# Kernel tuning notes

Measured on AMD Instinct MI355X. Metric: run time of the kernel, lower is better.

## Reference

```python
import jax, jax.numpy as jnp
import numpy as np

# Dimensions
T = 1024      # tokens
D = 1024      # d_model
DFF = 1024    # expert intermediate dim
R = 64        # tucker rank (r_in == r_out)
G = 8         # n_group
E = 32        # experts_per_group
NEXP = G * E  # 256 routed experts
K = 8         # top-k


def setup_inputs() -> dict:
    key = jax.random.key(0)
    ks = jax.random.split(key, 12)
    s = 0.02
    return {
        "x": jax.random.normal(ks[0], (T, D), jnp.float32),
        "Wg": jax.random.normal(ks[1], (D, NEXP), jnp.float32) * s,
        "uin_gate": jax.random.normal(ks[2], (G, D, R), jnp.float32) * s,
        "core_gate": jax.random.normal(ks[3], (G, E, R, R), jnp.float32) * s,
        "uout_gate": jax.random.normal(ks[4], (G, R, DFF), jnp.float32) * s,
        "uin_up": jax.random.normal(ks[5], (G, D, R), jnp.float32) * s,
        "core_up": jax.random.normal(ks[6], (G, E, R, R), jnp.float32) * s,
        "uout_up": jax.random.normal(ks[7], (G, R, DFF), jnp.float32) * s,
        "uin_down": jax.random.normal(ks[8], (G, DFF, R), jnp.float32) * s,
        "core_down": jax.random.normal(ks[9], (G, E, R, R), jnp.float32) * s,
        "uout_down": jax.random.normal(ks[10], (G, R, D), jnp.float32) * s,
    }


def _moe_forward(x, Wg, uin_gate, core_gate, uout_gate,
                 uin_up, core_up, uout_up,
                 uin_down, core_down, uout_down):
    Tn, d = x.shape
    # Router: top-k over 256 experts, softmax over the k logits (fp32 as in torch)
    logits = x @ Wg                                   # [T, NEXP]
    w, sel = jax.lax.top_k(logits, K)                 # [T, K]
    w = jax.nn.softmax(w.astype(jnp.float32), axis=-1).astype(x.dtype)

    e = sel.reshape(-1)                               # [F] global expert id
    g = e // E                                        # [F] group id
    tok = jnp.repeat(jnp.arange(Tn), K)               # [F] source token id
    mask = (g[:, None] == jnp.arange(G)[None, :]).astype(x.dtype)  # [F, G]

    def gather_in(uin):
        # project tokens with every group's u_in once, then gather per pair
        pre = jnp.einsum('td,gdr->gtr', x, uin)       # [G, T, R]
        return pre[g, tok]                            # [F, R]

    def core_apply(xin, core):
        # per-pair Tucker core slice bmm: x.unsqueeze(1) @ core[rel_idx]
        slices = core.reshape(G * E, R, R)[e]         # [F, R, R] gather
        return jnp.einsum('fr,fro->fo', xin, slices)  # [F, R]

    def group_out(h, U):
        # per-pair group-specific projection: h[f] @ U[g_f]
        out = jnp.zeros((h.shape[0], U.shape[-1]), h.dtype)
        for gi in range(G):  # fixed small loop over 8 groups
            out = out + (h * mask[:, gi:gi + 1]) @ U[gi]
        return out

    gate_h = group_out(core_apply(gather_in(uin_gate), core_gate), uout_gate)  # [F, DFF]
    up_h = group_out(core_apply(gather_in(uin_up), core_up), uout_up)          # [F, DFF]
    act = jax.nn.silu(gate_h) * up_h                                           # SwiGLU
    xin_d = group_out(act, uin_down)                                           # [F, R]
    out_f = group_out(core_apply(xin_d, core_down), uout_down)                 # [F, D]
    out_f = out_f * w.reshape(-1)[:, None]
    # scatter-add expert outputs back to tokens
    return jax.ops.segment_sum(out_f, tok, num_segments=Tn)


def reference(x, Wg, uin_gate, core_gate, uout_gate,
              uin_up, core_up, uout_up,
              uin_down, core_down, uout_down):
    return _moe_forward(x, Wg, uin_gate, core_gate, uout_gate,
                        uin_up, core_up, uout_up,
                        uin_down, core_down, uout_down)
```

## Files before the change

### kernel.cpp

```cpp
#include <hip/hip_runtime.h>
#include <hip/hip_bf16.h>
#include <math.h>


#define T_ 1024
#define D_ 1024
#define DFF_ 1024
#define R_ 64
#define G_ 8
#define E_ 32
#define NEXP_ 256
#define K_ 8
#define F_ 8192
#define LKZ_ 4
#define LTB_ 8
#define PKZ_ 2
#define DKZ_ 4
#define LP_ 72

typedef short bf16x8 __attribute__((ext_vector_type(8)));
typedef float f32x4 __attribute__((ext_vector_type(4)));

__device__ __forceinline__ unsigned short f2bf(float f) {
  unsigned int u = __float_as_uint(f);
  u += 0x7fffu + ((u >> 16) & 1u);
  return (unsigned short)(u >> 16);
}

__device__ __forceinline__ void stage_tile(short* dst, const unsigned short* src,
                                           int gp, int tid) {
  for (int idx = tid; idx < 512; idx += 256) {
    int r = idx >> 3, c8 = (idx & 7) << 3;
    *(uint4*)&dst[r * LP_ + c8] = *(const uint4*)&src[(size_t)r * gp + c8];
  }
}

__device__ __forceinline__ void stage_tile_guard(short* dst, const unsigned short* src,
                                                 int gp, int rows_valid, int tid) {
  for (int idx = tid; idx < 512; idx += 256) {
    int r = idx >> 3, c8 = (idx & 7) << 3;
    uint4 v = make_uint4(0u, 0u, 0u, 0u);
    if (r < rows_valid) v = *(const uint4*)&src[(size_t)r * gp + c8];
    *(uint4*)&dst[r * LP_ + c8] = v;
  }
}

__device__ __forceinline__ void stage_tile_f32(short* dst, const float* src,
                                               int gp, int tid) {
  for (int idx = tid; idx < 512; idx += 256) {
    int r = idx >> 3, c8 = (idx & 7) << 3;
    const float* s = &src[(size_t)r * gp + c8];
    float4 v0 = *(const float4*)s;
    float4 v1 = *(const float4*)(s + 4);
    uint4 u;
    u.x = ((unsigned)f2bf(v0.y) << 16) | f2bf(v0.x);
    u.y = ((unsigned)f2bf(v0.w) << 16) | f2bf(v0.z);
    u.z = ((unsigned)f2bf(v1.y) << 16) | f2bf(v1.x);
    u.w = ((unsigned)f2bf(v1.w) << 16) | f2bf(v1.z);
    *(uint4*)&dst[r * LP_ + c8] = u;
  }
}

__device__ __forceinline__ void mma_strip(const short* As, const short* Bs,
                                          int ms, int lane, f32x4* acc) {
  int lm = lane & 15;
  int lk = (lane >> 4) << 3;
#pragma unroll
  for (int kc = 0; kc < 64; kc += 32) {
    bf16x8 a = *(const bf16x8*)&As[(ms + lm) * LP_ + kc + lk];
#pragma unroll
    for (int nt = 0; nt < 4; ++nt) {
      bf16x8 b = *(const bf16x8*)&Bs[(nt * 16 + lm) * LP_ + kc + lk];
      acc[nt] = __builtin_amdgcn_mfma_f32_16x16x32_bf16(a, b, acc[nt], 0, 0, 0);
    }
  }
}

__global__ __launch_bounds__(256) void k_prep_logits(
    const float* __restrict__ x, const float* __restrict__ Wg,
    const float* __restrict__ s0, const float* __restrict__ s1,
    const float* __restrict__ s2, const float* __restrict__ s3,
    const float* __restrict__ s4, const float* __restrict__ s5,
    unsigned short* __restrict__ xb,
    unsigned short* __restrict__ d0, unsigned short* __restrict__ d1,
    unsigned short* __restrict__ d2, unsigned short* __restrict__ d3,
    unsigned short* __restrict__ d4, unsigned short* __restrict__ d5,
    int* __restrict__ cnt, int* __restrict__ tickets, float* __restrict__ Yf,
    float* __restrict__ lp) {
  __shared__ float shbuf[64 * 65];
  int b = blockIdx.x;
  if (b < 512) {
    int t0 = (b & 127) * LTB_;
    int z = b >> 7;
    int e = threadIdx.x;
    float* xs = shbuf;
    float a[LTB_] = {};
    int dc = z * 256;
    {
      int idx = threadIdx.x * 8;
      int tl = idx >> 8, d = idx & 255;
      *(float4*)&xs[tl * 256 + d] = *(const float4*)&x[(size_t)(t0 + tl) * D_ + dc + d];
      *(float4*)&xs[tl * 256 + d + 4] = *(const float4*)&x[(size_t)(t0 + tl) * D_ + dc + d + 4];
    }
    __syncthreads();
#pragma unroll 2
    for (int d2 = 0; d2 < 256; d2 += 4) {
      float w0 = Wg[(size_t)(dc + d2 + 0) * NEXP_ + e];
      float w1 = Wg[(size_t)(dc + d2 + 1) * NEXP_ + e];
      float w2 = Wg[(size_t)(dc + d2 + 2) * NEXP_ + e];
      float w3 = Wg[(size_t)(dc + d2 + 3) * NEXP_ + e];
#pragma unroll
      for (int j = 0; j < LTB_; ++j) {
        float4 xv = *(const float4*)&xs[j * 256 + d2];
        float aj = a[j];
        aj = fmaf(xv.x, w0, aj);
        aj = fmaf(xv.y, w1, aj);
        aj = fmaf(xv.z, w2, aj);
        aj = fmaf(xv.w, w3, aj);
        a[j] = aj;
      }
    }
    size_t base = (size_t)z * T_ * NEXP_;
#pragma unroll
    for (int j = 0; j < LTB_; ++j)
      lp[base + (size_t)(t0 + j) * NEXP_ + e] = a[j];
    return;
  }
  int b2 = b - 512;
  int id = b2 >> 7, rem = b2 & 127, g = rem >> 4, tile = rem & 15;
  if (id == 6) {
    size_t base = ((size_t)g * 16 + tile) * 8192;
    for (int i = threadIdx.x; i < 2048; i += 256) {
      size_t idx = base + (size_t)i * 4;
      float4 v = *(const float4*)&x[idx];
      xb[idx + 0] = f2bf(v.x);
      xb[idx + 1] = f2bf(v.y);
      xb[idx + 2] = f2bf(v.z);
      xb[idx + 3] = f2bf(v.w);
    }
    size_t ybase = ((size_t)g * 16 + tile) * 4096;
    float4 z4 = make_float4(0.f, 0.f, 0.f, 0.f);
    for (int i = threadIdx.x; i < 1024; i += 256)
      *(float4*)&Yf[ybase + (size_t)i * 4] = z4;
    if (g == 0 && tile == 0) {
      cnt[threadIdx.x] = 0;
      if (threadIdx.x == 0) tickets[0] = 0;
    }
    return;
  }
  const float* src = id == 0 ? s0 : id == 1 ? s1 : id == 2 ? s2 : id == 3 ? s3 : id == 4 ? s4 : s5;
  unsigned short* dst = id == 0 ? d0 : id == 1 ? d1 : id == 2 ? d2 : id == 3 ? d3 : id == 4 ? d4 : d5;
  if (id < 3) {
    int r0 = tile * 64;
    for (int idx = threadIdx.x; idx < 4096; idx += 256) {
      int r = idx >> 6, c = idx & 63;
      shbuf[r * 65 + c] = src[((size_t)g * 1024 + r0 + r) * 64 + c];
    }
    __syncthreads();
    for (int idx = threadIdx.x; idx < 4096; idx += 256) {
      int c = idx >> 6, r = idx & 63;
      dst[((size_t)g * 64 + c) * 1024 + r0 + r] = f2bf(shbuf[r * 65 + c]);
    }
  } else {
    int c0 = tile * 64;
    for (int idx = threadIdx.x; idx < 4096; idx += 256) {
      int r = idx >> 6, c = idx & 63;
      shbuf[r * 65 + c] = src[((size_t)g * 64 + r) * 1024 + c0 + c];
    }
    __syncthreads();
    if (id == 5) {
      for (int idx = threadIdx.x; idx < 4096; idx += 256) {
        int c = idx >> 6, r = idx & 63;
        dst[(size_t)(c0 + c) * 512 + g * 64 + r] = f2bf(shbuf[r * 65 + c]);
      }
    } else {
      for (int idx = threadIdx.x; idx < 4096; idx += 256) {
        int c = idx >> 6, r = idx & 63;
        dst[((size_t)g * 1024 + c0 + c) * 64 + r] = f2bf(shbuf[r * 65 + c]);
      }
    }
  }
}

__global__ __launch_bounds__(256) void k_pre_topk(
    const unsigned short* __restrict__ xb,
    const unsigned short* __restrict__ uinT_g, const unsigned short* __restrict__ uinT_u,
    const float* __restrict__ lp,
    float* __restrict__ Pgp, float* __restrict__ Pup,
    float* __restrict__ wsm, int* __restrict__ bucket, int* __restrict__ cnt,
    int* __restrict__ tickets, int* __restrict__ off) {
  __shared__ short sh2[2 * 64 * LP_];
  __shared__ int lastfl;
  int b = blockIdx.x;
  int tid = threadIdx.x;
  if (b >= 256) {
    int b2 = b - 256;
    int tile = b2 & 15, g = (b2 >> 4) & 7, zz = b2 >> 7;
    int gu = zz >> 1, kz = zz & 1;
    const unsigned short* U = gu ? uinT_u : uinT_g;
    float* P = gu ? Pup : Pgp;
    int t0 = tile * 64;
    short* As = sh2;
    short* Bs = sh2 + 64 * LP_;
    int lane = tid & 63, ms = (tid >> 6) * 16;
    f32x4 acc[4] = {};
    int dlo = kz * (D_ / PKZ_);
    for (int dc = dlo; dc < dlo + D_ / PKZ_; dc += 64) {
      stage_tile(As, xb + (size_t)t0 * D_ + dc, D_, tid);
      stage_tile(Bs, U + (size_t)g * 64 * 1024 + dc, 1024, tid);
      __syncthreads();
      mma_strip(As, Bs, ms, lane, acc);
      __syncthreads();
    }
    int lm = lane & 15, lq = (lane >> 4) * 4;
#pragma unroll
    for (int nt = 0; nt < 4; ++nt)
#pragma unroll
      for (int r = 0; r < 4; ++r)
        P[((size_t)(kz * G_ + g) * T_ + t0 + ms + lq + r) * R_ + nt * 16 + lm] = acc[nt][r];
    return;
  }
  int wave = tid >> 6;
  int lane = tid & 63;
  int t = b * 4 + wave;
  float v[4];
  int idx[4];
#pragma unroll
  for (int j = 0; j < 4; ++j) {
    idx[j] = lane + 64 * j;
    float s = 0.f;
#pragma unroll
    for (int z = 0; z < LKZ_; ++z)
      s += lp[(size_t)z * T_ * NEXP_ + (size_t)t * NEXP_ + idx[j]];
    v[j] = s;
  }
  float topv[K_];
  int topi[K_];
#pragma unroll
  for (int k = 0; k < K_; ++k) {
    float bv = v[0];
    int bi = idx[0];
#pragma unroll
    for (int j = 1; j < 4; ++j)
      if (v[j] > bv || (v[j] == bv && idx[j] < bi)) { bv = v[j]; bi = idx[j]; }
#pragma unroll
    for (int o2 = 32; o2 > 0; o2 >>= 1) {
      float ov = __shfl_xor(bv, o2);
      int oi = __shfl_xor(bi, o2);
      if (ov > bv || (ov == bv && oi < bi)) { bv = ov; bi = oi; }
    }
    topv[k] = bv;
    topi[k] = bi;
#pragma unroll
    for (int j = 0; j < 4; ++j)
      if (idx[j] == bi) v[j] = -INFINITY;
  }
  float m = topv[0];
  float ev[K_];
  float s = 0.f;
#pragma unroll
  for (int k = 0; k < K_; ++k) { ev[k] = expf(topv[k] - m); s += ev[k]; }
  float inv = 1.f / s;
  if (lane < K_) {
    wsm[t * K_ + lane] = ev[lane] * inv;
    int r1 = atomicAdd(&cnt[topi[lane]], 1);
    bucket[topi[lane] * 1024 + r1] = t * K_ + lane;
  }
  __threadfence();
  __syncthreads();
  if (tid == 0) lastfl = (atomicAdd(&tickets[0], 1) == 255) ? 1 : 0;
  __syncthreads();
  if (lastfl) {
    int* sarr = (int*)sh2;
    int i = tid;
    int c0 = atomicAdd(&cnt[i], 0);
    sarr[i] = c0;
    __syncthreads();
    for (int d = 1; d < NEXP_; d <<= 1) {
      int vv = (i >= d) ? sarr[i - d] : 0;
      __syncthreads();
      sarr[i] += vv;
      __syncthreads();
    }
    off[i + 1] = sarr[i];
    if (i == 0) off[0] = 0;
  }
}

__global__ __launch_bounds__(256) void k_core_gu(const float* __restrict__ Pgp,
                                                 const float* __restrict__ Pup,
                                                 const float* __restrict__ core_g,
                                                 const float* __restrict__ core_u,
                                                 const int* __restrict__ bucket,
                                                 const int* __restrict__ off,
                                                 unsigned short* __restrict__ xgb,
                                                 unsigned short* __restrict__ xub) {
  int e = blockIdx.x >> 1, half = blockIdx.x & 1;
  int g = e >> 5;
  __shared__ float cg[4096], cu[4096];
  __shared__ float rg[4][64], ru[4][64];
  int tid = threadIdx.x;
  for (int i = tid; i < 1024; i += 256) {
    *(float4*)&cg[i * 4] = *(const float4*)&core_g[(size_t)e * 4096 + (size_t)i * 4];
    *(float4*)&cu[i * 4] = *(const float4*)&core_u[(size_t)e * 4096 + (size_t)i * 4];
  }
  int p0 = off[e], n = off[e + 1] - p0;
  if (n < 0) n = 0;
  if (n > 1024) n = 1024;
  int hn = (n + 1) >> 1;
  int i0 = half * hn;
  int i1 = i0 + hn; if (i1 > n) i1 = n;
  int pl = tid >> 6, o = tid & 63;
  __syncthreads();
  for (int ib = i0; ib < i1; ib += 4) {
    int i = ib + pl;
    bool valid = i < i1;
    int p = p0 + i;
    float sg = 0.f, su = 0.f;
    if (valid) {
      int t = bucket[e * 1024 + i] >> 3;
#pragma unroll
      for (int kz = 0; kz < PKZ_; ++kz) {
        sg += Pgp[((size_t)(kz * G_ + g) * T_ + t) * R_ + o];
        su += Pup[((size_t)(kz * G_ + g) * T_ + t) * R_ + o];
      }
    }
    __syncthreads();
    rg[pl][o] = sg;
    ru[pl][o] = su;
    __syncthreads();
    if (valid) {
      float ag = 0.f, au = 0.f;
#pragma unroll 8
      for (int r = 0; r < R_; ++r) {
        ag = fmaf(rg[pl][r], cg[r * R_ + o], ag);
        au = fmaf(ru[pl][r], cu[r * R_ + o], au);
      }
      xgb[(size_t)p * R_ + o] = f2bf(ag);
      xub[(size_t)p * R_ + o] = f2bf(au);
    }
  }
}

__global__ __launch_bounds__(256) void k_fused_ad(const unsigned short* __restrict__ xgb,
                                                  const unsigned short* __restrict__ xub,
                                                  const unsigned short* __restrict__ uoutT_g,
                                                  const unsigned short* __restrict__ uoutT_u,
                                                  const unsigned short* __restrict__ uinT_d,
                                                  const int* __restrict__ off,
                                                  float* __restrict__ xdp) {
  int g = blockIdx.y;
  int kz = blockIdx.z;
  int p0 = off[g * E_];
  int pend = off[g * E_ + E_];
  if (p0 < 0) p0 = 0;
  if (pend > F_) pend = F_;
  if (pend < p0) pend = p0;
  int ntiles = (pend - p0 + 63) >> 6;
  __shared__ short Ag[64 * LP_], Au[64 * LP_];
  __shared__ short Bg[64 * LP_], Bu[64 * LP_], Bd[64 * LP_];
  __shared__ short Pt[64 * LP_];
  int tid = threadIdx.x, lane = tid & 63, ms = (tid >> 6) * 16;
  int lm = lane & 15, lq = (lane >> 4) * 4;
  for (int tile = blockIdx.x; tile < ntiles; tile += gridDim.x) {
    int pbase = p0 + tile * 64;
    int rv = pend - pbase; if (rv > 64) rv = 64;
    stage_tile_guard(Ag, xgb + (size_t)pbase * R_, R_, rv, tid);
    stage_tile_guard(Au, xub + (size_t)pbase * R_, R_, rv, tid);
    f32x4 accd[4] = {};
#pragma unroll
    for (int c4 = 0; c4 < 4; ++c4) {
      int cc = kz * (DFF_ / DKZ_) + c4 * 64;
      stage_tile(Bg, uoutT_g + ((size_t)g * DFF_ + cc) * R_, R_, tid);
      stage_tile(Bu, uoutT_u + ((size_t)g * DFF_ + cc) * R_, R_, tid);
      stage_tile(Bd, uinT_d + (size_t)g * 64 * 1024 + cc, 1024, tid);
      __syncthreads();
      f32x4 accg[4] = {}, accu[4] = {};
      mma_strip(Ag, Bg, ms, lane, accg);
      mma_strip(Au, Bu, ms, lane, accu);
#pragma unroll
      for (int nt = 0; nt < 4; ++nt)
#pragma unroll
        for (int r = 0; r < 4; ++r) {
          float gv = accg[nt][r];
          float av = gv / (1.f + expf(-gv)) * accu[nt][r];
          Pt[(ms + lq + r) * LP_ + nt * 16 + lm] = (short)f2bf(av);
        }
      mma_strip(Pt, Bd, ms, lane, accd);
      __syncthreads();
    }
#pragma unroll
    for (int nt = 0; nt < 4; ++nt)
#pragma unroll
      for (int r = 0; r < 4; ++r) {
        int p = pbase + ms + lq + r;
        if (p < pend) xdp[((size_t)kz * F_ + p) * R_ + nt * 16 + lm] = accd[nt][r];
      }
    __syncthreads();
  }
}

__global__ __launch_bounds__(256) void k_down_core(const float* __restrict__ xdp,
                                                   const float* __restrict__ core_d,
                                                   const int* __restrict__ bucket,
                                                   const float* __restrict__ wsm,
                                                   const int* __restrict__ off,
                                                   float* __restrict__ Yf) {
  int e = blockIdx.x >> 1, half = blockIdx.x & 1;
  int g = e >> 5;
  __shared__ float cd[4096];
  __shared__ float xs[4][64];
  int tid = threadIdx.x;
  for (int i = tid; i < 1024; i += 256)
    *(float4*)&cd[i * 4] = *(const float4*)&core_d[(size_t)e * 4096 + (size_t)i * 4];
  int p0 = off[e], n = off[e + 1] - p0;
  if (n < 0) n = 0;
  if (n > 1024) n = 1024;
  int hn = (n + 1) >> 1;
  int i0 = half * hn;
  int i1 = i0 + hn; if (i1 > n) i1 = n;
  int pl = tid >> 6, o = tid & 63;
  __syncthreads();
  for (int ib = i0; ib < i1; ib += 4) {
    int i = ib + pl;
    bool valid = i < i1;
    int p = p0 + i;
    int f = valid ? bucket[e * 1024 + i] : 0;
    float s = 0.f;
    if (valid) {
#pragma unroll
      for (int kz = 0; kz < DKZ_; ++kz) s += xdp[((size_t)kz * F_ + p) * R_ + o];
    }
    __syncthreads();
    xs[pl][o] = s;
    __syncthreads();
    if (valid) {
      float a = 0.f;
#pragma unroll 8
      for (int r = 0; r < R_; ++r) a = fmaf(xs[pl][r], cd[r * R_ + o], a);
      atomicAdd(&Yf[(size_t)(f >> 3) * 512 + g * 64 + o], wsm[f] * a);
    }
  }
}

__global__ __launch_bounds__(256) void k_fin(const float* __restrict__ Yf,
                                             const unsigned short* __restrict__ Uod2T,
                                             float* __restrict__ out) {
  int t0 = blockIdx.x * 64;
  int d0 = blockIdx.y * 64;
  __shared__ short As[64 * LP_], Bs[64 * LP_];
  __shared__ float Os[64 * 68];
  int tid = threadIdx.x, lane = tid & 63, ms = (tid >> 6) * 16;
  int lm = lane & 15, lq = (lane >> 4) * 4;
  f32x4 acc[4] = {};
  for (int kc = 0; kc < 512; kc += 64) {
    stage_tile_f32(As, Yf + (size_t)t0 * 512 + kc, 512, tid);
    stage_tile(Bs, Uod2T + (size_t)d0 * 512 + kc, 512, tid);
    __syncthreads();
    mma_strip(As, Bs, ms, lane, acc);
    __syncthreads();
  }
#pragma unroll
  for (int nt = 0; nt < 4; ++nt)
#pragma unroll
    for (int r = 0; r < 4; ++r)
      Os[(ms + lq + r) * 68 + nt * 16 + lm] = acc[nt][r];
  __syncthreads();
  for (int idx = tid; idx < 1024; idx += 256) {
    int r = idx >> 4, c4 = (idx & 15) << 2;
    *(float4*)&out[(size_t)(t0 + r) * D_ + d0 + c4] = *(const float4*)&Os[r * 68 + c4];
  }
}

extern "C" void kernel_launch(void* const* d_in, const int* in_sizes, int n_in,
                              void* d_out, int out_size, void* d_ws, size_t ws_size,
                              hipStream_t stream) {
  const float* x = (const float*)d_in[0];
  const float* Wg = (const float*)d_in[1];
  const float* uin_gate = (const float*)d_in[2];
  const float* core_gate = (const float*)d_in[3];
  const float* uout_gate = (const float*)d_in[4];
  const float* uin_up = (const float*)d_in[5];
  const float* core_up = (const float*)d_in[6];
  const float* uout_up = (const float*)d_in[7];
  const float* uin_down = (const float*)d_in[8];
  const float* core_down = (const float*)d_in[9];
  const float* uout_down = (const float*)d_in[10];
  float* out = (float*)d_out;

  char* ws = (char*)d_ws;
  size_t o = 0;
  auto alloc = [&](size_t bytes) { size_t r = o; o = (o + bytes + 255) & ~(size_t)255; return r; };
  size_t o_lp = alloc((size_t)LKZ_ * T_ * NEXP_ * 4);
  size_t o_wsm = alloc(F_ * 4);
  size_t o_bucket = alloc((size_t)NEXP_ * 1024 * 4);
  size_t o_cnt = alloc(NEXP_ * 4);
  size_t o_tickets = alloc(256);
  size_t o_off = alloc((NEXP_ + 1) * 4);
  size_t o_xb = alloc((size_t)T_ * D_ * 2);
  size_t o_uinT_g = alloc((size_t)G_ * 64 * 1024 * 2);
  size_t o_uinT_u = alloc((size_t)G_ * 64 * 1024 * 2);
  size_t o_uinT_d = alloc((size_t)G_ * 64 * 1024 * 2);
  size_t o_uoutT_g = alloc((size_t)G_ * 1024 * 64 * 2);
  size_t o_uoutT_u = alloc((size_t)G_ * 1024 * 64 * 2);
  size_t o_Uod2T = alloc((size_t)D_ * 512 * 2);
  size_t o_xgb = alloc((size_t)F_ * R_ * 2);
  size_t o_xub = alloc((size_t)F_ * R_ * 2);
  size_t o_Y = alloc((size_t)T_ * 512 * 4);
  size_t o_pgp = alloc((size_t)PKZ_ * G_ * T_ * R_ * 4);
  size_t o_pup = alloc((size_t)PKZ_ * G_ * T_ * R_ * 4);
  size_t o_xdp = alloc((size_t)DKZ_ * F_ * R_ * 4);
  (void)ws_size;

  float* lp = (float*)(ws + o_lp);
  float* wsm = (float*)(ws + o_wsm);
  int* bucket = (int*)(ws + o_bucket);
  int* cnt = (int*)(ws + o_cnt);
  int* tickets = (int*)(ws + o_tickets);
  int* off = (int*)(ws + o_off);
  unsigned short* xb = (unsigned short*)(ws + o_xb);
  unsigned short* uinT_g = (unsigned short*)(ws + o_uinT_g);
  unsigned short* uinT_u = (unsigned short*)(ws + o_uinT_u);
  unsigned short* uinT_d = (unsigned short*)(ws + o_uinT_d);
  unsigned short* uoutT_g = (unsigned short*)(ws + o_uoutT_g);
  unsigned short* uoutT_u = (unsigned short*)(ws + o_uoutT_u);
  unsigned short* Uod2T = (unsigned short*)(ws + o_Uod2T);
  unsigned short* xgb = (unsigned short*)(ws + o_xgb);
  unsigned short* xub = (unsigned short*)(ws + o_xub);
  float* Yf = (float*)(ws + o_Y);
  float* pgp = (float*)(ws + o_pgp);
  float* pup = (float*)(ws + o_pup);
  float* xdp = (float*)(ws + o_xdp);

  k_prep_logits<<<1408, 256, 0, stream>>>(x, Wg, uin_gate, uin_up, uin_down,
                                          uout_gate, uout_up, uout_down, xb,
                                          uinT_g, uinT_u, uinT_d,
                                          uoutT_g, uoutT_u, Uod2T,
                                          cnt, tickets, Yf, lp);
  k_pre_topk<<<768, 256, 0, stream>>>(xb, uinT_g, uinT_u, lp, pgp, pup,
                                      wsm, bucket, cnt, tickets, off);
  k_core_gu<<<NEXP_ * 2, 256, 0, stream>>>(pgp, pup, core_gate, core_up, bucket, off, xgb, xub);
  k_fused_ad<<<dim3(16, G_, DKZ_), 256, 0, stream>>>(xgb, xub, uoutT_g, uoutT_u, uinT_d, off, xdp);
  k_down_core<<<NEXP_ * 2, 256, 0, stream>>>(xdp, core_down, bucket, wsm, off, Yf);
  k_fin<<<dim3(16, 16), 256, 0, stream>>>(Yf, Uod2T, out);
}
```

Before: 223.5 us.

## Double-buffer LDS tiles using direct global-to-LDS async loads in GEMM kernels

Replaces the register-staged global→LDS tile copies with `__builtin_amdgcn_global_load_lds` direct loads in three kernels: the pre-top-k projection, the fused gate/up/down kernel and the final down projection. Each kernel now double-buffers its tiles so the next tile is fetched while MFMAs run on the current one, with one barrier per iteration instead of two. The LDS row padding (stride 72) is dropped to a plain 64 stride, because the direct-load layout requires contiguous per-wave writes. This may bring back LDS bank conflicts on the bf16x8 reads and the Pt writes. Out-of-range rows are now clamped to the last valid row instead of zero-filled.

Measured after the change: 222.7 us. Within noise of the previous version (-0.3%).

```diff
diff --git a/kernel.cpp b/kernel.cpp
--- a/kernel.cpp
+++ b/kernel.cpp
@@ -16,7 +16,6 @@
 #define LTB_ 8
 #define PKZ_ 2
 #define DKZ_ 4
-#define LP_ 72
 
 typedef short bf16x8 __attribute__((ext_vector_type(8)));
 typedef float f32x4 __attribute__((ext_vector_type(4)));
@@ -27,38 +26,32 @@
   return (unsigned short)(u >> 16);
 }
 
-__device__ __forceinline__ void stage_tile(short* dst, const unsigned short* src,
-                                           int gp, int tid) {
-  for (int idx = tid; idx < 512; idx += 256) {
-    int r = idx >> 3, c8 = (idx & 7) << 3;
-    *(uint4*)&dst[r * LP_ + c8] = *(const uint4*)&src[(size_t)r * gp + c8];
-  }
-}
-
-__device__ __forceinline__ void stage_tile_guard(short* dst, const unsigned short* src,
-                                                 int gp, int rows_valid, int tid) {
-  for (int idx = tid; idx < 512; idx += 256) {
-    int r = idx >> 3, c8 = (idx & 7) << 3;
-    uint4 v = make_uint4(0u, 0u, 0u, 0u);
-    if (r < rows_valid) v = *(const uint4*)&src[(size_t)r * gp + c8];
-    *(uint4*)&dst[r * LP_ + c8] = v;
-  }
-}
-
-__device__ __forceinline__ void stage_tile_f32(short* dst, const float* src,
-                                               int gp, int tid) {
-  for (int idx = tid; idx < 512; idx += 256) {
-    int r = idx >> 3, c8 = (idx & 7) << 3;
-    const float* s = &src[(size_t)r * gp + c8];
-    float4 v0 = *(const float4*)s;
-    float4 v1 = *(const float4*)(s + 4);
-    uint4 u;
-    u.x = ((unsigned)f2bf(v0.y) << 16) | f2bf(v0.x);
-    u.y = ((unsigned)f2bf(v0.w) << 16) | f2bf(v0.z);
-    u.z = ((unsigned)f2bf(v1.y) << 16) | f2bf(v1.x);
-    u.w = ((unsigned)f2bf(v1.w) << 16) | f2bf(v1.z);
-    *(uint4*)&dst[r * LP_ + c8] = u;
-  }
+typedef const __attribute__((address_space(1))) unsigned int guint;
+typedef __attribute__((address_space(3))) unsigned int luint;
+
+__device__ __forceinline__ void gstage(short* lds, const unsigned short* src,
+                                       int gp, int tid) {
+  int w = tid >> 6, l = tid & 63;
+  int r0 = (w << 4) + (l >> 3);
+  int c = (l & 7) << 3;
+  __builtin_amdgcn_global_load_lds((guint*)&src[(size_t)r0 * gp + c],
+                                   (luint*)&lds[w << 10], 16, 0, 0);
+  __builtin_amdgcn_global_load_lds((guint*)&src[(size_t)(r0 + 8) * gp + c],
+                                   (luint*)&lds[(w << 10) + 512], 16, 0, 0);
+}
+
+__device__ __forceinline__ void gstage_clamp(short* lds, const unsigned short* src,
+                                             int gp, int rows_valid, int tid) {
+  int w = tid >> 6, l = tid & 63;
+  int c = (l & 7) << 3;
+  int r0 = (w << 4) + (l >> 3);
+  int r1 = r0 + 8;
+  if (r0 >= rows_valid) r0 = rows_valid - 1;
+  if (r1 >= rows_valid) r1 = rows_valid - 1;
+  __builtin_amdgcn_global_load_lds((guint*)&src[(size_t)r0 * gp + c],
+                                   (luint*)&lds[w << 10], 16, 0, 0);
+  __builtin_amdgcn_global_load_lds((guint*)&src[(size_t)r1 * gp + c],
+                                   (luint*)&lds[(w << 10) + 512], 16, 0, 0);
 }
 
 __device__ __forceinline__ void mma_strip(const short* As, const short* Bs,
@@ -67,13 +60,37 @@
   int lk = (lane >> 4) << 3;
 #pragma unroll
   for (int kc = 0; kc < 64; kc += 32) {
-    bf16x8 a = *(const bf16x8*)&As[(ms + lm) * LP_ + kc + lk];
+    bf16x8 a = *(const bf16x8*)&As[(ms + lm) * 64 + kc + lk];
 #pragma unroll
     for (int nt = 0; nt < 4; ++nt) {
-      bf16x8 b = *(const bf16x8*)&Bs[(nt * 16 + lm) * LP_ + kc + lk];
+      bf16x8 b = *(const bf16x8*)&Bs[(nt * 16 + lm) * 64 + kc + lk];
       acc[nt] = __builtin_amdgcn_mfma_f32_16x16x32_bf16(a, b, acc[nt], 0, 0, 0);
     }
   }
+}
+
+__device__ __forceinline__ void a_load(float4* pre, const float* src, int gp, int tid) {
+  int r = tid >> 2, c = (tid & 3) << 4;
+  const float* s = &src[(size_t)r * gp + c];
+  pre[0] = *(const float4*)(s + 0);
+  pre[1] = *(const float4*)(s + 4);
+  pre[2] = *(const float4*)(s + 8);
+  pre[3] = *(const float4*)(s + 12);
+}
+
+__device__ __forceinline__ void a_write(short* dst, const float4* pre, int tid) {
+  int r = tid >> 2, c = (tid & 3) << 4;
+  uint4 u0, u1;
+  u0.x = ((unsigned)f2bf(pre[0].y) << 16) | f2bf(pre[0].x);
+  u0.y = ((unsigned)f2bf(pre[0].w) << 16) | f2bf(pre[0].z);
+  u0.z = ((unsigned)f2bf(pre[1].y) << 16) | f2bf(pre[1].x);
+  u0.w = ((unsigned)f2bf(pre[1].w) << 16) | f2bf(pre[1].z);
+  u1.x = ((unsigned)f2bf(pre[2].y) << 16) | f2bf(pre[2].x);
+  u1.y = ((unsigned)f2bf(pre[2].w) << 16) | f2bf(pre[2].z);
+  u1.z = ((unsigned)f2bf(pre[3].y) << 16) | f2bf(pre[3].x);
+  u1.w = ((unsigned)f2bf(pre[3].w) << 16) | f2bf(pre[3].z);
+  *(uint4*)&dst[r * 64 + c] = u0;
+  *(uint4*)&dst[r * 64 + c + 8] = u1;
 }
 
 __global__ __launch_bounds__(256) void k_prep_logits(
@@ -189,7 +206,7 @@
     float* __restrict__ Pgp, float* __restrict__ Pup,
     float* __restrict__ wsm, int* __restrict__ bucket, int* __restrict__ cnt,
     int* __restrict__ tickets, int* __restrict__ off) {
-  __shared__ short sh2[2 * 64 * LP_];
+  __shared__ __align__(16) short sh[4][4096];
   __shared__ int lastfl;
   int b = blockIdx.x;
   int tid = threadIdx.x;
@@ -200,17 +217,25 @@
     const unsigned short* U = gu ? uinT_u : uinT_g;
     float* P = gu ? Pup : Pgp;
     int t0 = tile * 64;
-    short* As = sh2;
-    short* Bs = sh2 + 64 * LP_;
     int lane = tid & 63, ms = (tid >> 6) * 16;
     f32x4 acc[4] = {};
     int dlo = kz * (D_ / PKZ_);
-    for (int dc = dlo; dc < dlo + D_ / PKZ_; dc += 64) {
-      stage_tile(As, xb + (size_t)t0 * D_ + dc, D_, tid);
-      stage_tile(Bs, U + (size_t)g * 64 * 1024 + dc, 1024, tid);
+    const unsigned short* Asrc = xb + (size_t)t0 * D_;
+    const unsigned short* Bsrc = U + (size_t)g * 64 * 1024;
+    gstage(sh[0], Asrc + dlo, D_, tid);
+    gstage(sh[2], Bsrc + dlo, 1024, tid);
+    __syncthreads();
+    int cur = 0;
+#pragma unroll 1
+    for (int i = 0; i < 8; ++i) {
+      if (i < 7) {
+        int dc = dlo + (i + 1) * 64;
+        gstage(sh[cur ^ 1], Asrc + dc, D_, tid);
+        gstage(sh[2 + (cur ^ 1)], Bsrc + dc, 1024, tid);
+      }
+      mma_strip(sh[cur], sh[2 + cur], ms, lane, acc);
       __syncthreads();
-      mma_strip(As, Bs, ms, lane, acc);
-      __syncthreads();
+      cur ^= 1;
     }
     int lm = lane & 15, lq = (lane >> 4) * 4;
 #pragma unroll
@@ -271,7 +296,7 @@
   if (tid == 0) lastfl = (atomicAdd(&tickets[0], 1) == 255) ? 1 : 0;
   __syncthreads();
   if (lastfl) {
-    int* sarr = (int*)sh2;
+    int* sarr = (int*)sh;
     int i = tid;
     int c0 = atomicAdd(&cnt[i], 0);
     sarr[i] = c0;
@@ -357,37 +382,47 @@
   if (pend > F_) pend = F_;
   if (pend < p0) pend = p0;
   int ntiles = (pend - p0 + 63) >> 6;
-  __shared__ short Ag[64 * LP_], Au[64 * LP_];
-  __shared__ short Bg[64 * LP_], Bu[64 * LP_], Bd[64 * LP_];
-  __shared__ short Pt[64 * LP_];
+  __shared__ __align__(16) short Ag[4096], Au[4096], Pt[4096];
+  __shared__ __align__(16) short Bg[2][4096], Bu[2][4096], Bd[2][4096];
   int tid = threadIdx.x, lane = tid & 63, ms = (tid >> 6) * 16;
   int lm = lane & 15, lq = (lane >> 4) * 4;
+  int cc0 = kz * (DFF_ / DKZ_);
+  const unsigned short* Bgsrc = uoutT_g + (size_t)g * DFF_ * R_;
+  const unsigned short* Busrc = uoutT_u + (size_t)g * DFF_ * R_;
+  const unsigned short* Bdsrc = uinT_d + (size_t)g * 64 * 1024;
   for (int tile = blockIdx.x; tile < ntiles; tile += gridDim.x) {
     int pbase = p0 + tile * 64;
     int rv = pend - pbase; if (rv > 64) rv = 64;
-    stage_tile_guard(Ag, xgb + (size_t)pbase * R_, R_, rv, tid);
-    stage_tile_guard(Au, xub + (size_t)pbase * R_, R_, rv, tid);
+    gstage_clamp(Ag, xgb + (size_t)pbase * R_, R_, rv, tid);
+    gstage_clamp(Au, xub + (size_t)pbase * R_, R_, rv, tid);
+    gstage(Bg[0], Bgsrc + (size_t)cc0 * R_, R_, tid);
+    gstage(Bu[0], Busrc + (size_t)cc0 * R_, R_, tid);
+    gstage(Bd[0], Bdsrc + cc0, 1024, tid);
+    __syncthreads();
     f32x4 accd[4] = {};
-#pragma unroll
+    int cur = 0;
+#pragma unroll 1
     for (int c4 = 0; c4 < 4; ++c4) {
-      int cc = kz * (DFF_ / DKZ_) + c4 * 64;
-      stage_tile(Bg, uoutT_g + ((size_t)g * DFF_ + cc) * R_, R_, tid);
-      stage_tile(Bu, uoutT_u + ((size_t)g * DFF_ + cc) * R_, R_, tid);
-      stage_tile(Bd, uinT_d + (size_t)g * 64 * 1024 + cc, 1024, tid);
-      __syncthreads();
+      if (c4 < 3) {
+        int cc = cc0 + (c4 + 1) * 64;
+        gstage(Bg[cur ^ 1], Bgsrc + (size_t)cc * R_, R_, tid);
+        gstage(Bu[cur ^ 1], Busrc + (size_t)cc * R_, R_, tid);
+        gstage(Bd[cur ^ 1], Bdsrc + cc, 1024, tid);
+      }
       f32x4 accg[4] = {}, accu[4] = {};
-      mma_strip(Ag, Bg, ms, lane, accg);
-      mma_strip(Au, Bu, ms, lane, accu);
+      mma_strip(Ag, Bg[cur], ms, lane, accg);
+      mma_strip(Au, Bu[cur], ms, lane, accu);
 #pragma unroll
       for (int nt = 0; nt < 4; ++nt)
 #pragma unroll
         for (int r = 0; r < 4; ++r) {
           float gv = accg[nt][r];
           float av = gv / (1.f + expf(-gv)) * accu[nt][r];
-          Pt[(ms + lq + r) * LP_ + nt * 16 + lm] = (short)f2bf(av);
+          Pt[(ms + lq + r) * 64 + nt * 16 + lm] = (short)f2bf(av);
         }
-      mma_strip(Pt, Bd, ms, lane, accd);
+      mma_strip(Pt, Bd[cur], ms, lane, accd);
       __syncthreads();
+      cur ^= 1;
     }
 #pragma unroll
     for (int nt = 0; nt < 4; ++nt)
@@ -448,18 +483,35 @@
                                              float* __restrict__ out) {
   int t0 = blockIdx.x * 64;
   int d0 = blockIdx.y * 64;
-  __shared__ short As[64 * LP_], Bs[64 * LP_];
-  __shared__ float Os[64 * 68];
+  __shared__ __align__(16) short sh[4][4096];
   int tid = threadIdx.x, lane = tid & 63, ms = (tid >> 6) * 16;
   int lm = lane & 15, lq = (lane >> 4) * 4;
+  const float* Asrc = Yf + (size_t)t0 * 512;
+  const unsigned short* Bsrc = Uod2T + (size_t)d0 * 512;
   f32x4 acc[4] = {};
-  for (int kc = 0; kc < 512; kc += 64) {
-    stage_tile_f32(As, Yf + (size_t)t0 * 512 + kc, 512, tid);
-    stage_tile(Bs, Uod2T + (size_t)d0 * 512 + kc, 512, tid);
-    __syncthreads();
-    mma_strip(As, Bs, ms, lane, acc);
-    __syncthreads();
-  }
+  {
+    float4 pre[4];
+    a_load(pre, Asrc, 512, tid);
+    a_write(sh[0], pre, tid);
+  }
+  gstage(sh[2], Bsrc, 512, tid);
+  __syncthreads();
+  int cur = 0;
+#pragma unroll 1
+  for (int i = 0; i < 8; ++i) {
+    float4 pre[4];
+    bool hp = i < 7;
+    if (hp) {
+      int kc = (i + 1) * 64;
+      a_load(pre, Asrc + kc, 512, tid);
+      gstage(sh[2 + (cur ^ 1)], Bsrc + kc, 512, tid);
+    }
+    mma_strip(sh[cur], sh[2 + cur], ms, lane, acc);
+    if (hp) a_write(sh[cur ^ 1], pre, tid);
+    __syncthreads();
+    cur ^= 1;
+  }
+  float* Os = (float*)sh;
 #pragma unroll
   for (int nt = 0; nt < 4; ++nt)
 #pragma unroll
```
